# Kernel optimization log

Measured on AMD Instinct MI355X. Metric: run time of the kernel, lower is better.

## Reference

```python
import jax, jax.numpy as jnp
import numpy as np

L, B, N, W, H = 8, 8, 1024, 768, 12
C = W // H  # per-head channel dim = 64


def setup_inputs() -> dict:
    key = jax.random.key(0)
    ks = jax.random.split(key, 5)
    s = 0.02  # init scale for weights
    return {
        "x": jax.random.normal(ks[0], (B, N, W), jnp.float32),
        "Wqkv": jax.random.normal(ks[1], (L, W, 3 * W), jnp.float32) * s,
        "bqkv": jnp.zeros((L, 3 * W), jnp.float32),
        "Wo": jax.random.normal(ks[2], (L, W, W), jnp.float32) * s,
        "bo": jnp.zeros((L, W), jnp.float32),
        "Wfc": jax.random.normal(ks[3], (L, W, 4 * W), jnp.float32) * s,
        "bfc": jnp.zeros((L, 4 * W), jnp.float32),
        "Wpr": jax.random.normal(ks[4], (L, 4 * W, W), jnp.float32) * s,
        "bpr": jnp.zeros((L, W), jnp.float32),
        "g1": jnp.ones((L, W), jnp.float32),
        "b1": jnp.zeros((L, W), jnp.float32),
        "g2": jnp.ones((L, W), jnp.float32),
        "b2": jnp.zeros((L, W), jnp.float32),
    }


def _ln(x, g, b, eps=1e-5):
    m = jnp.mean(x, axis=-1, keepdims=True)
    v = jnp.var(x, axis=-1, keepdims=True)
    return (x - m) * jax.lax.rsqrt(v + eps) * g + b


def reference(x, Wqkv, bqkv, Wo, bo, Wfc, bfc, Wpr, bpr, g1, b1, g2, b2):
    scale = 1.0 / np.sqrt(np.sqrt(C))  # applied to BOTH q and k, as in source

    def block(h, p):
        wqkv, bq, wo, bo_, wfc, bf, wpr, bp, G1, B1, G2, B2 = p
        # --- attention ---
        y = _ln(h, G1, B1)
        qkv = y @ wqkv + bq                       # [B,N,3W]
        qkv = qkv.reshape(B, N, H, 3 * C)         # per-head interleaved q|k|v
        q, k, v = jnp.split(qkv, 3, axis=-1)      # each [B,N,H,C]
        w = jnp.einsum('bthc,bshc->bhts', q * scale, k * scale)
        w = jax.nn.softmax(w.astype(jnp.float32), axis=-1).astype(w.dtype)
        attn = jnp.einsum('bhts,bshc->bthc', w, v).reshape(B, N, W)
        h = h + attn @ wo + bo_
        # --- MLP (exact GELU, matching torch F.gelu default) ---
        y2 = _ln(h, G2, B2)
        h = h + jax.nn.gelu(y2 @ wfc + bf, approximate=False) @ wpr + bp
        return h, None

    out, _ = jax.lax.scan(block, x, (Wqkv, bqkv, Wo, bo, Wfc, bfc, Wpr, bpr, g1, b1, g2, b2))
    return out
```

## Files before the change

### kernel.cpp

```cpp
#include <hip/hip_runtime.h>
#include <hip/hip_bf16.h>
#include <cstdint>
#include <cstddef>


typedef __attribute__((ext_vector_type(8))) short bf16x8;
typedef __attribute__((ext_vector_type(4))) float f32x4;

#define MFMA16(a, b, c) __builtin_amdgcn_mfma_f32_16x16x32_bf16((a), (b), (c), 0, 0, 0)

__device__ __forceinline__ void gld_lds16(const void* g, void* l) {
    __builtin_amdgcn_global_load_lds((const __attribute__((address_space(1))) unsigned int*)g,
                                     (__attribute__((address_space(3))) unsigned int*)l,
                                     16, 0, 0);
}

__device__ __forceinline__ unsigned short f32_to_bf16_bits(float f) {
    unsigned u = __builtin_bit_cast(unsigned, f);
    u += 0x7fffu + ((u >> 16) & 1u);
    return (unsigned short)(u >> 16);
}

__device__ __forceinline__ unsigned pack_bf2(float a, float b) {
    return (unsigned)f32_to_bf16_bits(a) | ((unsigned)f32_to_bf16_bits(b) << 16);
}

__device__ __forceinline__ unsigned cvt_pk_bf16(float lo, float hi) {
    unsigned r;
    asm("v_cvt_pk_bf16_f32 %0, %1, %2" : "=v"(r) : "v"(lo), "v"(hi));
    return r;
}

template <bool GELU>
__global__ __launch_bounds__(512, 2) void gemm256(const __hip_bfloat16* __restrict__ A,
                                                  const __hip_bfloat16* __restrict__ Bt,
                                                  const float* __restrict__ bias,
                                                  __hip_bfloat16* __restrict__ outh,
                                                  int N, int K) {
    __shared__ __hip_bfloat16 lA[2][256 * 64];
    __shared__ __hip_bfloat16 lB[2][256 * 64];
    const int t = threadIdx.x;
    const int w = t >> 6, l = t & 63;
    const int lr = l & 15, lg = l >> 4;
    const int wr = w >> 2, wc = w & 3;
    const int bid = blockIdx.x;
    const int xcd = bid & 7, local = bid >> 3;
    const int m0 = (xcd * 4 + (local & 3)) * 256;
    const int n0 = (local >> 2) * 256;

    const int srow = t >> 3, sslot = t & 7;
#define STAGE_A(buf, kt)                                                            \
    {                                                                               \
        _Pragma("unroll") for (int j = 0; j < 4; j++) {                             \
            const int row = srow + j * 64;                                          \
            gld_lds16(&A[(size_t)(m0 + row) * K + (kt) * 64 + ((sslot ^ (row & 7)) << 3)], \
                      &lA[buf][(t + j * 512) * 8]);                                 \
        }                                                                           \
    }
#define STAGE_B(buf, kt)                                                            \
    {                                                                               \
        _Pragma("unroll") for (int j = 0; j < 4; j++) {                             \
            const int row = srow + j * 64;                                          \
            gld_lds16(&Bt[(size_t)(n0 + row) * K + (kt) * 64 + ((sslot ^ (row & 7)) << 3)], \
                      &lB[buf][(t + j * 512) * 8]);                                 \
        }                                                                           \
    }

    f32x4 acc[8][4];
#pragma unroll
    for (int i = 0; i < 8; i++)
#pragma unroll
        for (int j = 0; j < 4; j++) acc[i][j] = (f32x4){0.f, 0.f, 0.f, 0.f};

    STAGE_A(0, 0);
    STAGE_B(0, 0);
    __syncthreads();

    const int NT = K >> 6;
    for (int kt = 0; kt < NT; ++kt) {
        const int cur = kt & 1;
        const bool more = (kt + 1 < NT);
        const __hip_bfloat16* sA = lA[cur];
        const __hip_bfloat16* sB = lB[cur];
        bf16x8 af[4][2], bf[4][2];

#pragma unroll
        for (int mt = 0; mt < 4; mt++)
#pragma unroll
            for (int ks = 0; ks < 2; ks++) {
                const int row = wr * 128 + mt * 16 + lr;
                af[mt][ks] = *(const bf16x8*)&sA[row * 64 + ((((ks << 2) | lg) ^ (row & 7)) << 3)];
            }
#pragma unroll
        for (int nt = 0; nt < 2; nt++)
#pragma unroll
            for (int ks = 0; ks < 2; ks++) {
                const int row = wc * 64 + nt * 16 + lr;
                bf[nt][ks] = *(const bf16x8*)&sB[row * 64 + ((((ks << 2) | lg) ^ (row & 7)) << 3)];
            }
        if (more) STAGE_A(cur ^ 1, kt + 1);
        __builtin_amdgcn_s_barrier();
        asm volatile("s_waitcnt lgkmcnt(0)" ::: "memory");
        __builtin_amdgcn_sched_barrier(0);
        __builtin_amdgcn_s_setprio(1);
#pragma unroll
        for (int mt = 0; mt < 4; mt++)
#pragma unroll
            for (int nt = 0; nt < 2; nt++)
#pragma unroll
                for (int ks = 0; ks < 2; ks++)
                    acc[mt][nt] = MFMA16(af[mt][ks], bf[nt][ks], acc[mt][nt]);
        __builtin_amdgcn_s_setprio(0);
        __builtin_amdgcn_s_barrier();

#pragma unroll
        for (int nt = 2; nt < 4; nt++)
#pragma unroll
            for (int ks = 0; ks < 2; ks++) {
                const int row = wc * 64 + nt * 16 + lr;
                bf[nt][ks] = *(const bf16x8*)&sB[row * 64 + ((((ks << 2) | lg) ^ (row & 7)) << 3)];
            }
        if (more) STAGE_B(cur ^ 1, kt + 1);
        __builtin_amdgcn_s_barrier();
        asm volatile("s_waitcnt lgkmcnt(0)" ::: "memory");
        __builtin_amdgcn_sched_barrier(0);
        __builtin_amdgcn_s_setprio(1);
#pragma unroll
        for (int mt = 0; mt < 4; mt++)
#pragma unroll
            for (int nt = 2; nt < 4; nt++)
#pragma unroll
                for (int ks = 0; ks < 2; ks++)
                    acc[mt][nt] = MFMA16(af[mt][ks], bf[nt][ks], acc[mt][nt]);
        __builtin_amdgcn_s_setprio(0);
        __builtin_amdgcn_s_barrier();

#pragma unroll
        for (int mt = 0; mt < 4; mt++)
#pragma unroll
            for (int ks = 0; ks < 2; ks++) {
                const int row = wr * 128 + 64 + mt * 16 + lr;
                af[mt][ks] = *(const bf16x8*)&sA[row * 64 + ((((ks << 2) | lg) ^ (row & 7)) << 3)];
            }
        __builtin_amdgcn_s_barrier();
        asm volatile("s_waitcnt lgkmcnt(0)" ::: "memory");
        __builtin_amdgcn_sched_barrier(0);
        __builtin_amdgcn_s_setprio(1);
#pragma unroll
        for (int mt = 0; mt < 4; mt++)
#pragma unroll
            for (int nt = 2; nt < 4; nt++)
#pragma unroll
                for (int ks = 0; ks < 2; ks++)
                    acc[4 + mt][nt] = MFMA16(af[mt][ks], bf[nt][ks], acc[4 + mt][nt]);
        __builtin_amdgcn_s_setprio(0);
        __builtin_amdgcn_s_barrier();

        __builtin_amdgcn_s_setprio(1);
#pragma unroll
        for (int mt = 0; mt < 4; mt++)
#pragma unroll
            for (int nt = 0; nt < 2; nt++)
#pragma unroll
                for (int ks = 0; ks < 2; ks++)
                    acc[4 + mt][nt] = MFMA16(af[mt][ks], bf[nt][ks], acc[4 + mt][nt]);
        __builtin_amdgcn_s_setprio(0);
        asm volatile("s_waitcnt vmcnt(0)" ::: "memory");
        __builtin_amdgcn_sched_barrier(0);
        __builtin_amdgcn_s_barrier();
    }
#undef STAGE_A
#undef STAGE_B

#pragma unroll
    for (int nt = 0; nt < 4; nt++) {
        const int col = n0 + wc * 64 + nt * 16 + lr;
        const float bv = bias[col];
#pragma unroll
        for (int mt = 0; mt < 8; mt++) {
#pragma unroll
            for (int r = 0; r < 4; r++) {
                const int row = m0 + wr * 128 + mt * 16 + lg * 4 + r;
                float v = acc[mt][nt][r] + bv;
                if (GELU) v = 0.5f * v * (1.f + erff(v * 0.70710678118654752f));
                outh[(size_t)row * N + col] = __float2bfloat16(v);
            }
        }
    }
}

template <bool RES, bool GELU, bool WF, bool WH>
__global__ __launch_bounds__(256) void gemm_bt(const __hip_bfloat16* __restrict__ A,
                                               const __hip_bfloat16* __restrict__ Bt,
                                               const float* __restrict__ bias,
                                               const float* __restrict__ res,
                                               float* __restrict__ outf,
                                               __hip_bfloat16* __restrict__ outh,
                                               int N, int K) {
    __shared__ __hip_bfloat16 lA0[128 * 32], lA1[128 * 32];
    __shared__ __hip_bfloat16 lB0[128 * 32], lB1[128 * 32];
    const int t = threadIdx.x;
    const int w = t >> 6, l = t & 63;
    const int lr = l & 15, lg = l >> 4;
    const int bid = blockIdx.x;
    const int xcd = bid & 7;
    const int local = bid >> 3;
    const int m0 = (xcd * 8 + (local & 7)) * 128;
    const int n0 = (local >> 3) * 128;
    const int wm = (w & 1) * 64, wn = (w >> 1) * 64;

    f32x4 acc[4][4];
#pragma unroll
    for (int i = 0; i < 4; i++)
#pragma unroll
        for (int j = 0; j < 4; j++) acc[i][j] = (f32x4){0.f, 0.f, 0.f, 0.f};

    for (int k0 = 0; k0 < K; k0 += 64) {
        __syncthreads();
#pragma unroll
        for (int i = 0; i < 2; i++) {
            int c = t + i * 256;
            int row = c >> 2, seg = c & 3;
            const size_t ab = (size_t)(m0 + row) * K + k0 + seg * 8;
            const size_t bb = (size_t)(n0 + row) * K + k0 + seg * 8;
            gld_lds16(&A[ab],       &lA0[c * 8]);
            gld_lds16(&A[ab + 32],  &lA1[c * 8]);
            gld_lds16(&Bt[bb],      &lB0[c * 8]);
            gld_lds16(&Bt[bb + 32], &lB1[c * 8]);
        }
        __syncthreads();
#pragma unroll
        for (int hh = 0; hh < 2; hh++) {
            const __hip_bfloat16* sA = hh ? lA1 : lA0;
            const __hip_bfloat16* sB = hh ? lB1 : lB0;
            bf16x8 af[4], bfr[4];
#pragma unroll
            for (int mt = 0; mt < 4; mt++)
                af[mt] = *(const bf16x8*)&sA[(wm + mt * 16 + lr) * 32 + lg * 8];
#pragma unroll
            for (int nt = 0; nt < 4; nt++)
                bfr[nt] = *(const bf16x8*)&sB[(wn + nt * 16 + lr) * 32 + lg * 8];
#pragma unroll
            for (int mt = 0; mt < 4; mt++)
#pragma unroll
                for (int nt = 0; nt < 4; nt++)
                    acc[mt][nt] = MFMA16(af[mt], bfr[nt], acc[mt][nt]);
        }
    }

#pragma unroll
    for (int nt = 0; nt < 4; nt++) {
        const int col = n0 + wn + nt * 16 + lr;
        const float bv = bias[col];
#pragma unroll
        for (int mt = 0; mt < 4; mt++) {
#pragma unroll
            for (int r = 0; r < 4; r++) {
                const int row = m0 + wm + mt * 16 + lg * 4 + r;
                const size_t idx = (size_t)row * N + col;
                float v = acc[mt][nt][r] + bv;
                if (RES) v += res[idx];
                if (GELU) v = 0.5f * v * (1.f + erff(v * 0.70710678118654752f));
                if (WF) outf[idx] = v;
                if (WH) outh[idx] = __float2bfloat16(v);
            }
        }
    }
}

__global__ __launch_bounds__(256) void ln_kernel(const float* __restrict__ h,
                                                 const float* __restrict__ g,
                                                 const float* __restrict__ b,
                                                 __hip_bfloat16* __restrict__ y) {
    const int t = threadIdx.x;
    const int w = t >> 6, l = t & 63;
    const int row = blockIdx.x * 4 + w;
    const float4* hr = (const float4*)(h + (size_t)row * 768);
    const float4* g4 = (const float4*)g;
    const float4* b4 = (const float4*)b;
    float4 x[3];
    float s = 0.f, q = 0.f;
#pragma unroll
    for (int j = 0; j < 3; j++) {
        x[j] = hr[l + j * 64];
        s += x[j].x + x[j].y + x[j].z + x[j].w;
        q += x[j].x * x[j].x + x[j].y * x[j].y + x[j].z * x[j].z + x[j].w * x[j].w;
    }
#pragma unroll
    for (int d = 1; d < 64; d <<= 1) {
        s += __shfl_xor(s, d);
        q += __shfl_xor(q, d);
    }
    const float mean = s * (1.f / 768.f);
    const float var = q * (1.f / 768.f) - mean * mean;
    const float rs = rsqrtf(var + 1e-5f);
    uint2* yr = (uint2*)(y + (size_t)row * 768);
#pragma unroll
    for (int j = 0; j < 3; j++) {
        const float4 gg = g4[l + j * 64], bb = b4[l + j * 64];
        float o0 = (x[j].x - mean) * rs * gg.x + bb.x;
        float o1 = (x[j].y - mean) * rs * gg.y + bb.y;
        float o2 = (x[j].z - mean) * rs * gg.z + bb.z;
        float o3 = (x[j].w - mean) * rs * gg.w + bb.w;
        yr[l + j * 64] = make_uint2(pack_bf2(o0, o1), pack_bf2(o2, o3));
    }
}

__global__ __launch_bounds__(256) void transpose_weights(const float* __restrict__ sq,
                                                         const float* __restrict__ so,
                                                         const float* __restrict__ sf,
                                                         const float* __restrict__ sp,
                                                         __hip_bfloat16* __restrict__ dq,
                                                         __hip_bfloat16* __restrict__ dO,
                                                         __hip_bfloat16* __restrict__ df,
                                                         __hip_bfloat16* __restrict__ dp) {
    const int bid = blockIdx.x;
    const float* src;
    __hip_bfloat16* dst;
    int K, N, tloc;
    if (bid < 1728)      { src = sq; dst = dq; K = 768;  N = 2304; tloc = bid; }
    else if (bid < 2304) { src = so; dst = dO; K = 768;  N = 768;  tloc = bid - 1728; }
    else if (bid < 4608) { src = sf; dst = df; K = 768;  N = 3072; tloc = bid - 2304; }
    else                 { src = sp; dst = dp; K = 3072; N = 768;  tloc = bid - 4608; }
    const int ktiles = K / 32;
    const int k0 = (tloc % ktiles) * 32;
    const int n0 = (tloc / ktiles) * 32;
    const int t = threadIdx.x;
    __shared__ float tile[32][33];
#pragma unroll
    for (int p = 0; p < 4; p++) {
        int rr = p * 8 + (t >> 5);
        tile[rr][t & 31] = src[(size_t)(k0 + rr) * N + n0 + (t & 31)];
    }
    __syncthreads();
#pragma unroll
    for (int p = 0; p < 4; p++) {
        int rr = p * 8 + (t >> 5);
        dst[(size_t)(n0 + rr) * K + k0 + (t & 31)] = __float2bfloat16(tile[t & 31][rr]);
    }
}

__global__ __launch_bounds__(256) void vt_transpose(const short* __restrict__ qkv,
                                                    short* __restrict__ vt) {
    const int bid = blockIdx.x;
    const int bh = bid >> 6, tau = bid & 63;
    const int b = bh / 12, h = bh % 12;
    const int ct = tau >> 5, nt = tau & 31;
    const int n0 = nt * 32, c0 = ct * 32;
    const int t = threadIdx.x;
    __shared__ short tile[32][33];
    const short* base = qkv + (size_t)(b * 1024 + n0) * 2304 + h * 192 + 128 + c0;
#pragma unroll
    for (int p = 0; p < 4; p++) {
        int rr = p * 8 + (t >> 5);
        tile[rr][t & 31] = base[(size_t)rr * 2304 + (t & 31)];
    }
    __syncthreads();
    short* ob = vt + (size_t)((b * 12 + h) * 64 + c0) * 1024 + n0;
#pragma unroll
    for (int p = 0; p < 4; p++) {
        int rr = p * 8 + (t >> 5);
        ob[(size_t)rr * 1024 + (t & 31)] = tile[t & 31][rr];
    }
}

__global__ __launch_bounds__(256) void attn_kernel(const short* __restrict__ qkv,
                                                   const short* __restrict__ vt,
                                                   short* __restrict__ attnout) {
    const int bid = blockIdx.x;
    const int xcd = bid & 7, j = bid >> 3;
    const int bh = xcd * 12 + (j >> 4);
    const int qt = j & 15;
    const int b = bh / 12, hh = bh % 12;
    const int t = threadIdx.x, w = t >> 6, l = t & 63;
    const int lr = l & 15, lg = l >> 4;
    const int x7 = lr & 7;
    __shared__ short lK[64 * 64];
    __shared__ short lV[64 * 64];
    __shared__ short lP[4][16 * 64];
    const int qw = qt * 64 + w * 16;

    bf16x8 bq[2];
#pragma unroll
    for (int ks = 0; ks < 2; ks++)
        bq[ks] = *(const bf16x8*)&qkv[(size_t)(b * 1024 + qw + lr) * 2304 + hh * 192 + ks * 32 + lg * 8];

    int col[2];
    col[0] = (lg ^ x7) * 8;
    col[1] = ((4 | lg) ^ x7) * 8;

    const int c0 = t, c1 = t + 256;
    const int r0 = c0 >> 3, r1 = c1 >> 3;
    const int s0 = (c0 & 7) ^ (r0 & 7), s1 = (c1 & 7) ^ (r1 & 7);
    const short* gK0 = qkv + (size_t)(b * 1024 + r0) * 2304 + hh * 192 + 64 + s0 * 8;
    const short* gK1 = qkv + (size_t)(b * 1024 + r1) * 2304 + hh * 192 + 64 + s1 * 8;
    const short* gV0 = vt + (size_t)((b * 12 + hh) * 64 + r0) * 1024 + s0 * 8;
    const short* gV1 = vt + (size_t)((b * 12 + hh) * 64 + r1) * 1024 + s1 * 8;

    f32x4 o[4];
#pragma unroll
    for (int dt = 0; dt < 4; dt++) o[dt] = (f32x4){0.f, 0.f, 0.f, 0.f};
    const float cexp = 0.125f * 1.44269504088896f;
    float cm = -1.0e30f;
    float lsum = 0.f;

    for (int kt = 0; kt < 16; kt++) {
        const int key0 = kt * 64;
        __syncthreads();
        gld_lds16(gK0 + (size_t)key0 * 2304, &lK[c0 * 8]);
        gld_lds16(gK1 + (size_t)key0 * 2304, &lK[c1 * 8]);
        gld_lds16(gV0 + key0, &lV[c0 * 8]);
        gld_lds16(gV1 + key0, &lV[c1 * 8]);
        __syncthreads();

        f32x4 s[4];
#pragma unroll
        for (int nt = 0; nt < 4; nt++) s[nt] = (f32x4){0.f, 0.f, 0.f, 0.f};
#pragma unroll
        for (int nt = 0; nt < 4; nt++)
#pragma unroll
            for (int ks = 0; ks < 2; ks++) {
                bf16x8 ak = *(const bf16x8*)&lK[(nt * 16 + lr) * 64 + col[ks]];
                s[nt] = MFMA16(ak, bq[ks], s[nt]);
            }

        float mx = s[0][0];
#pragma unroll
        for (int nt = 0; nt < 4; nt++)
#pragma unroll
            for (int r = 0; r < 4; r++) mx = fmaxf(mx, s[nt][r]);
        mx = fmaxf(mx, __shfl_xor(mx, 16));
        mx = fmaxf(mx, __shfl_xor(mx, 32));
        const float tm = mx * cexp;
        if (!__all(tm <= cm + 8.f)) {
            const float cmn = fmaxf(cm, tm);
            const float alpha = exp2f(cm - cmn);
            cm = cmn;
            lsum *= alpha;
            float af[4];
#pragma unroll
            for (int r = 0; r < 4; r++) af[r] = __shfl(alpha, lg * 4 + r);
#pragma unroll
            for (int dt = 0; dt < 4; dt++)
#pragma unroll
                for (int r = 0; r < 4; r++) o[dt][r] *= af[r];
        }
        float ps = 0.f;
#pragma unroll
        for (int nt = 0; nt < 4; nt++)
#pragma unroll
            for (int r = 0; r < 4; r++) {
                float p = exp2f(s[nt][r] * cexp - cm);
                s[nt][r] = p;
                ps += p;
            }
        ps += __shfl_xor(ps, 16);
        ps += __shfl_xor(ps, 32);
        lsum += ps;

#pragma unroll
        for (int nt = 0; nt < 4; nt++) {
            unsigned pk0 = cvt_pk_bf16(s[nt][0], s[nt][1]);
            unsigned pk1 = cvt_pk_bf16(s[nt][2], s[nt][3]);
            const int S = nt * 2 + (lg >> 1);
            *(uint2*)&lP[w][lr * 64 + ((S ^ x7) << 3) + ((lg & 1) << 2)] = make_uint2(pk0, pk1);
        }

#pragma unroll
        for (int kc = 0; kc < 2; kc++) {
            bf16x8 ap = *(const bf16x8*)&lP[w][lr * 64 + col[kc]];
#pragma unroll
            for (int dt = 0; dt < 4; dt++) {
                bf16x8 bv = *(const bf16x8*)&lV[(dt * 16 + lr) * 64 + col[kc]];
                o[dt] = MFMA16(ap, bv, o[dt]);
            }
        }
    }

    float inv[4];
#pragma unroll
    for (int r = 0; r < 4; r++) inv[r] = 1.f / __shfl(lsum, lg * 4 + r);
#pragma unroll
    for (int dt = 0; dt < 4; dt++)
#pragma unroll
        for (int r = 0; r < 4; r++)
            attnout[(size_t)(b * 1024 + qw + lg * 4 + r) * 768 + hh * 64 + dt * 16 + lr] =
                (short)f32_to_bf16_bits(o[dt][r] * inv[r]);
}

extern "C" void kernel_launch(void* const* d_in, const int* in_sizes, int n_in,
                              void* d_out, int out_size, void* d_ws, size_t ws_size,
                              hipStream_t stream) {
    const float* x    = (const float*)d_in[0];
    const float* Wqkv = (const float*)d_in[1];
    const float* bqkv = (const float*)d_in[2];
    const float* Wo   = (const float*)d_in[3];
    const float* bo   = (const float*)d_in[4];
    const float* Wfc  = (const float*)d_in[5];
    const float* bfc  = (const float*)d_in[6];
    const float* Wpr  = (const float*)d_in[7];
    const float* bpr  = (const float*)d_in[8];
    const float* g1   = (const float*)d_in[9];
    const float* b1   = (const float*)d_in[10];
    const float* g2   = (const float*)d_in[11];
    const float* b2   = (const float*)d_in[12];
    float* h = (float*)d_out;

    char* ws = (char*)d_ws;
    size_t off = 0;
    auto alloc = [&](size_t bytes) -> void* {
        void* p = ws + off;
        off += (bytes + 255) & ~(size_t)255;
        return p;
    };
    __hip_bfloat16* tQKV = (__hip_bfloat16*)alloc((size_t)2304 * 768 * 2);
    __hip_bfloat16* tO   = (__hip_bfloat16*)alloc((size_t)768 * 768 * 2);
    __hip_bfloat16* tFC  = (__hip_bfloat16*)alloc((size_t)3072 * 768 * 2);
    __hip_bfloat16* tPR  = (__hip_bfloat16*)alloc((size_t)768 * 3072 * 2);
    __hip_bfloat16* y    = (__hip_bfloat16*)alloc((size_t)8192 * 768 * 2);
    __hip_bfloat16* att  = (__hip_bfloat16*)alloc((size_t)8192 * 768 * 2);
    __hip_bfloat16* vtb  = (__hip_bfloat16*)alloc((size_t)8192 * 768 * 2);
    __hip_bfloat16* big  = (__hip_bfloat16*)alloc((size_t)8192 * 3072 * 2);
    __hip_bfloat16* qkvb = big;
    __hip_bfloat16* fcb  = big;

    hipMemcpyAsync(h, x, (size_t)8 * 1024 * 768 * 4, hipMemcpyDeviceToDevice, stream);

    for (int L = 0; L < 8; L++) {
        const float* wq = Wqkv + (size_t)L * 768 * 2304;
        const float* wo = Wo   + (size_t)L * 768 * 768;
        const float* wf = Wfc  + (size_t)L * 768 * 3072;
        const float* wp = Wpr  + (size_t)L * 3072 * 768;

        transpose_weights<<<6912, 256, 0, stream>>>(wq, wo, wf, wp, tQKV, tO, tFC, tPR);

        ln_kernel<<<2048, 256, 0, stream>>>(h, g1 + L * 768, b1 + L * 768, y);

        gemm256<false><<<288, 512, 0, stream>>>(y, tQKV, bqkv + L * 2304, qkvb, 2304, 768);

        vt_transpose<<<6144, 256, 0, stream>>>((const short*)qkvb, (short*)vtb);

        attn_kernel<<<1536, 256, 0, stream>>>(
            (const short*)qkvb, (const short*)vtb, (short*)att);

        gemm_bt<true, false, true, false><<<6 * 64, 256, 0, stream>>>(
            att, tO, bo + L * 768, h, h, nullptr, 768, 768);

        ln_kernel<<<2048, 256, 0, stream>>>(h, g2 + L * 768, b2 + L * 768, y);

        gemm256<true><<<384, 512, 0, stream>>>(y, tFC, bfc + L * 3072, fcb, 3072, 768);

        gemm_bt<true, false, true, false><<<6 * 64, 256, 0, stream>>>(
            fcb, tPR, bpr + L * 768, h, h, nullptr, 768, 3072);
    }
}
```

Measured before the change: 2.593 ms.

## Split 256-tile GEMM staging into half-tiles with finer-grained vmcnt pipelining

Splits the A and B shared-memory tiles of the 256x256 GEMM into two 128-row halves. Each half is loaded in a separate phase of the k-loop, and the kernel waits with partial vmcnt counts instead of draining all loads at the end of each iteration. Warp-to-tile mapping changes so each warp covers interleaved 64-row/32-col slices across both halves, and the epilogue indexing is updated to match. The aim is to overlap global-to-LDS loads with MFMA work more continuously, at the cost of more complex wait/barrier ordering that must stay correct.

```diff
diff --git a/kernel.cpp b/kernel.cpp
--- a/kernel.cpp
+++ b/kernel.cpp
@@ -37,33 +37,36 @@
                                                   const float* __restrict__ bias,
                                                   __hip_bfloat16* __restrict__ outh,
                                                   int N, int K) {
-    __shared__ __hip_bfloat16 lA[2][256 * 64];
-    __shared__ __hip_bfloat16 lB[2][256 * 64];
+    __shared__ __hip_bfloat16 lA[2][2 * 128 * 64];
+    __shared__ __hip_bfloat16 lB[2][2 * 128 * 64];
     const int t = threadIdx.x;
     const int w = t >> 6, l = t & 63;
     const int lr = l & 15, lg = l >> 4;
     const int wr = w >> 2, wc = w & 3;
+    const int x7 = lr & 7;
+    const int cs0 = ((lg) ^ x7) << 3;
+    const int cs1 = ((4 | lg) ^ x7) << 3;
     const int bid = blockIdx.x;
     const int xcd = bid & 7, local = bid >> 3;
     const int m0 = (xcd * 4 + (local & 3)) * 256;
     const int n0 = (local >> 2) * 256;
 
     const int srow = t >> 3, sslot = t & 7;
-#define STAGE_A(buf, kt)                                                            \
-    {                                                                               \
-        _Pragma("unroll") for (int j = 0; j < 4; j++) {                             \
-            const int row = srow + j * 64;                                          \
+#define STAGE_A(buf, kt, hf)                                                          \
+    {                                                                                 \
+        _Pragma("unroll") for (int j = 0; j < 2; j++) {                               \
+            const int row = (hf) * 128 + srow + j * 64;                               \
             gld_lds16(&A[(size_t)(m0 + row) * K + (kt) * 64 + ((sslot ^ (row & 7)) << 3)], \
-                      &lA[buf][(t + j * 512) * 8]);                                 \
-        }                                                                           \
-    }
-#define STAGE_B(buf, kt)                                                            \
-    {                                                                               \
-        _Pragma("unroll") for (int j = 0; j < 4; j++) {                             \
-            const int row = srow + j * 64;                                          \
+                      &lA[buf][(hf) * 8192 + (t + j * 512) * 8]);                     \
+        }                                                                             \
+    }
+#define STAGE_B(buf, kt, hf)                                                          \
+    {                                                                                 \
+        _Pragma("unroll") for (int j = 0; j < 2; j++) {                               \
+            const int row = (hf) * 128 + srow + j * 64;                               \
             gld_lds16(&Bt[(size_t)(n0 + row) * K + (kt) * 64 + ((sslot ^ (row & 7)) << 3)], \
-                      &lB[buf][(t + j * 512) * 8]);                                 \
-        }                                                                           \
+                      &lB[buf][(hf) * 8192 + (t + j * 512) * 8]);                     \
+        }                                                                             \
     }
 
     f32x4 acc[8][4];
@@ -72,9 +75,13 @@
 #pragma unroll
         for (int j = 0; j < 4; j++) acc[i][j] = (f32x4){0.f, 0.f, 0.f, 0.f};
 
-    STAGE_A(0, 0);
-    STAGE_B(0, 0);
-    __syncthreads();
+    STAGE_A(0, 0, 0);
+    STAGE_B(0, 0, 0);
+    STAGE_B(0, 0, 1);
+    STAGE_A(0, 0, 1);
+    asm volatile("s_waitcnt vmcnt(4)" ::: "memory");
+    __builtin_amdgcn_sched_barrier(0);
+    __builtin_amdgcn_s_barrier();
 
     const int NT = K >> 6;
     for (int kt = 0; kt < NT; ++kt) {
@@ -85,20 +92,18 @@
         bf16x8 af[4][2], bf[4][2];
 
 #pragma unroll
-        for (int mt = 0; mt < 4; mt++)
-#pragma unroll
-            for (int ks = 0; ks < 2; ks++) {
-                const int row = wr * 128 + mt * 16 + lr;
-                af[mt][ks] = *(const bf16x8*)&sA[row * 64 + ((((ks << 2) | lg) ^ (row & 7)) << 3)];
-            }
-#pragma unroll
-        for (int nt = 0; nt < 2; nt++)
-#pragma unroll
-            for (int ks = 0; ks < 2; ks++) {
-                const int row = wc * 64 + nt * 16 + lr;
-                bf[nt][ks] = *(const bf16x8*)&sB[row * 64 + ((((ks << 2) | lg) ^ (row & 7)) << 3)];
-            }
-        if (more) STAGE_A(cur ^ 1, kt + 1);
+        for (int mt = 0; mt < 4; mt++) {
+            const int ro = (wr * 64 + mt * 16 + lr) * 64;
+            af[mt][0] = *(const bf16x8*)&sA[ro + cs0];
+            af[mt][1] = *(const bf16x8*)&sA[ro + cs1];
+        }
+#pragma unroll
+        for (int nt = 0; nt < 2; nt++) {
+            const int ro = (wc * 32 + nt * 16 + lr) * 64;
+            bf[nt][0] = *(const bf16x8*)&sB[ro + cs0];
+            bf[nt][1] = *(const bf16x8*)&sB[ro + cs1];
+        }
+        if (more) STAGE_A(cur ^ 1, kt + 1, 0);
         __builtin_amdgcn_s_barrier();
         asm volatile("s_waitcnt lgkmcnt(0)" ::: "memory");
         __builtin_amdgcn_sched_barrier(0);
@@ -111,16 +116,18 @@
                 for (int ks = 0; ks < 2; ks++)
                     acc[mt][nt] = MFMA16(af[mt][ks], bf[nt][ks], acc[mt][nt]);
         __builtin_amdgcn_s_setprio(0);
+        if (more) { asm volatile("s_waitcnt vmcnt(4)" ::: "memory"); }
+        else      { asm volatile("s_waitcnt vmcnt(2)" ::: "memory"); }
+        __builtin_amdgcn_sched_barrier(0);
         __builtin_amdgcn_s_barrier();
 
 #pragma unroll
-        for (int nt = 2; nt < 4; nt++)
-#pragma unroll
-            for (int ks = 0; ks < 2; ks++) {
-                const int row = wc * 64 + nt * 16 + lr;
-                bf[nt][ks] = *(const bf16x8*)&sB[row * 64 + ((((ks << 2) | lg) ^ (row & 7)) << 3)];
-            }
-        if (more) STAGE_B(cur ^ 1, kt + 1);
+        for (int nt = 2; nt < 4; nt++) {
+            const int ro = 8192 + (wc * 32 + (nt - 2) * 16 + lr) * 64;
+            bf[nt][0] = *(const bf16x8*)&sB[ro + cs0];
+            bf[nt][1] = *(const bf16x8*)&sB[ro + cs1];
+        }
+        if (more) STAGE_B(cur ^ 1, kt + 1, 0);
         __builtin_amdgcn_s_barrier();
         asm volatile("s_waitcnt lgkmcnt(0)" ::: "memory");
         __builtin_amdgcn_sched_barrier(0);
@@ -133,15 +140,18 @@
                 for (int ks = 0; ks < 2; ks++)
                     acc[mt][nt] = MFMA16(af[mt][ks], bf[nt][ks], acc[mt][nt]);
         __builtin_amdgcn_s_setprio(0);
+        if (more) { asm volatile("s_waitcnt vmcnt(4)" ::: "memory"); }
+        else      { asm volatile("s_waitcnt vmcnt(0)" ::: "memory"); }
+        __builtin_amdgcn_sched_barrier(0);
         __builtin_amdgcn_s_barrier();
 
 #pragma unroll
-        for (int mt = 0; mt < 4; mt++)
-#pragma unroll
-            for (int ks = 0; ks < 2; ks++) {
-                const int row = wr * 128 + 64 + mt * 16 + lr;
-                af[mt][ks] = *(const bf16x8*)&sA[row * 64 + ((((ks << 2) | lg) ^ (row & 7)) << 3)];
-            }
+        for (int mt = 0; mt < 4; mt++) {
+            const int ro = 8192 + (wr * 64 + mt * 16 + lr) * 64;
+            af[mt][0] = *(const bf16x8*)&sA[ro + cs0];
+            af[mt][1] = *(const bf16x8*)&sA[ro + cs1];
+        }
+        if (more) STAGE_B(cur ^ 1, kt + 1, 1);
         __builtin_amdgcn_s_barrier();
         asm volatile("s_waitcnt lgkmcnt(0)" ::: "memory");
         __builtin_amdgcn_sched_barrier(0);
@@ -154,8 +164,8 @@
                 for (int ks = 0; ks < 2; ks++)
                     acc[4 + mt][nt] = MFMA16(af[mt][ks], bf[nt][ks], acc[4 + mt][nt]);
         __builtin_amdgcn_s_setprio(0);
-        __builtin_amdgcn_s_barrier();
-
+
+        if (more) STAGE_A(cur ^ 1, kt + 1, 1);
         __builtin_amdgcn_s_setprio(1);
 #pragma unroll
         for (int mt = 0; mt < 4; mt++)
@@ -165,7 +175,7 @@
                 for (int ks = 0; ks < 2; ks++)
                     acc[4 + mt][nt] = MFMA16(af[mt][ks], bf[nt][ks], acc[4 + mt][nt]);
         __builtin_amdgcn_s_setprio(0);
-        asm volatile("s_waitcnt vmcnt(0)" ::: "memory");
+        if (more) { asm volatile("s_waitcnt vmcnt(4)" ::: "memory"); }
         __builtin_amdgcn_sched_barrier(0);
         __builtin_amdgcn_s_barrier();
     }
@@ -174,16 +184,16 @@
 
 #pragma unroll
     for (int nt = 0; nt < 4; nt++) {
-        const int col = n0 + wc * 64 + nt * 16 + lr;
+        const int col = n0 + ((nt < 2) ? (wc * 32 + nt * 16) : (128 + wc * 32 + (nt - 2) * 16)) + lr;
         const float bv = bias[col];
 #pragma unroll
         for (int mt = 0; mt < 8; mt++) {
+            const int rbase = m0 + ((mt < 4) ? (wr * 64 + mt * 16) : (128 + wr * 64 + (mt - 4) * 16)) + lg * 4;
 #pragma unroll
             for (int r = 0; r < 4; r++) {
-                const int row = m0 + wr * 128 + mt * 16 + lg * 4 + r;
                 float v = acc[mt][nt][r] + bv;
                 if (GELU) v = 0.5f * v * (1.f + erff(v * 0.70710678118654752f));
-                outh[(size_t)row * N + col] = __float2bfloat16(v);
+                outh[(size_t)(rbase + r) * N + col] = __float2bfloat16(v);
             }
         }
     }
```

Result: no change. 2.585 ms (-0.3%).
